# Optimization experiments

Measured on AMD Instinct MI355X. Metric: run time of the kernel, lower is better.

## Reference

```python
import jax, jax.numpy as jnp
import numpy as np

B, C, H, W = 4, 256, 224, 224
WH = WW = 8
SH = SW = 4
HEADS = 8
HD = C // HEADS
N = WH * WW
EPS = 1e-5


def _rel_index():
    coords = np.stack(np.meshgrid(np.arange(WH), np.arange(WW), indexing='ij')).reshape(2, -1)
    rel = (coords[:, :, None] - coords[:, None, :]).transpose(1, 2, 0).copy()
    rel[:, :, 0] += WH - 1
    rel[:, :, 1] += WW - 1
    rel[:, :, 0] *= 2 * WW - 1
    return rel.sum(-1)  # (N, N) int

REL_INDEX = _rel_index()


def _shift_mask(Hp, Wp):
    # Swin shift mask for one image: (nW, N, N) float, 0 or -100
    img = np.zeros((Hp, Wp))
    cnt = 0
    for a, b in [(0, Hp - WH), (Hp - WH, Hp - SH), (Hp - SH, Hp)]:
        for c, d in [(0, Wp - WW), (Wp - WW, Wp - SW), (Wp - SW, Wp)]:
            img[a:b, c:d] = cnt
            cnt += 1
    mw = img.reshape(Hp // WH, WH, Wp // WW, WW).transpose(0, 2, 1, 3).reshape(-1, N)
    diff = mw[:, None, :] - mw[:, :, None]  # [w, i, j] = mw[w,j] - mw[w,i]
    return np.where(diff != 0, np.float32(-100.0), np.float32(0.0)).astype(np.float32)


def _ln(x, w, b):
    m = jnp.mean(x, axis=-1, keepdims=True)
    v = jnp.mean(jnp.square(x - m), axis=-1, keepdims=True)
    return (x - m) * jax.lax.rsqrt(v + EPS) * w + b


def setup_inputs() -> dict:
    key = jax.random.key(0)
    ks = jax.random.split(key, 8)
    num_rel = (2 * WH - 1) * (2 * WW - 1)
    return {
        'x': jax.random.normal(ks[0], (B, C, H, W), dtype=jnp.float32),
        'qkv_w': jax.random.normal(ks[1], (3 * C, C), dtype=jnp.float32) * 0.02,
        'proj_w': jax.random.normal(ks[2], (C, C), dtype=jnp.float32) * 0.02,
        'proj_b': jnp.zeros((C,), dtype=jnp.float32),
        'rpb_table': jax.random.normal(ks[3], (num_rel, HEADS), dtype=jnp.float32) * 0.02,
        'norm1_w': jnp.ones((C,), dtype=jnp.float32),
        'norm1_b': jnp.zeros((C,), dtype=jnp.float32),
        'norm2_w': jnp.ones((C,), dtype=jnp.float32),
        'norm2_b': jnp.zeros((C,), dtype=jnp.float32),
        'mlp_w1': jax.random.normal(ks[4], (4 * C, C), dtype=jnp.float32) * 0.02,
        'mlp_b1': jnp.zeros((4 * C,), dtype=jnp.float32),
        'mlp_w2': jax.random.normal(ks[5], (C, 4 * C), dtype=jnp.float32) * 0.02,
        'mlp_b2': jnp.zeros((C,), dtype=jnp.float32),
    }


def reference(x, qkv_w, proj_w, proj_b, rpb_table, norm1_w, norm1_b,
              norm2_w, norm2_b, mlp_w1, mlp_b1, mlp_w2, mlp_b2):
    Bx, Cx, Hx, Wx = x.shape
    pad_h = (WH - Hx % WH) % WH
    pad_w = (WW - Wx % WW) % WW
    if pad_h or pad_w:
        x = jnp.pad(x, ((0, 0), (0, 0), (0, pad_h), (0, pad_w)))
    Hp, Wp = Hx + pad_h, Wx + pad_w
    x = jnp.transpose(x, (0, 2, 3, 1))                    # BHWC
    x = jnp.roll(x, (-SH, -SW), axis=(1, 2))
    nW = (Hp // WH) * (Wp // WW)
    # window partition -> (B*nW, N, C), batch-major
    xw = x.reshape(Bx, Hp // WH, WH, Wp // WW, WW, Cx)
    xw = jnp.transpose(xw, (0, 1, 3, 2, 4, 5)).reshape(-1, N, Cx)

    # ----- windowed attention -----
    h = _ln(xw, norm1_w, norm1_b)
    qkv = (h @ qkv_w.T).reshape(-1, N, 3, HEADS, HD)
    qkv = jnp.transpose(qkv, (2, 0, 3, 1, 4))             # (3, Bw, heads, N, hd)
    q, k, v = qkv[0], qkv[1], qkv[2]
    attn = jnp.einsum('bhnd,bhmd->bhnm', q, k) * (1.0 / HD ** 0.5)
    bias = jnp.transpose(rpb_table[REL_INDEX.reshape(-1)].reshape(N, N, HEADS), (2, 0, 1))
    attn = attn + bias[None]
    # faithful to torch: repeat_interleave(B, dim=0) -> window-major mask ordering
    mask = jnp.asarray(_shift_mask(Hp, Wp))               # (nW, N, N)
    attn = attn + jnp.repeat(mask, Bx, axis=0)[:, None]
    attn = jax.nn.softmax(attn, axis=-1)
    out = jnp.einsum('bhnm,bhmd->bhnd', attn, v)
    out = jnp.transpose(out, (0, 2, 1, 3)).reshape(-1, N, Cx)
    out = out @ proj_w.T + proj_b
    xw = xw + out

    # ----- MLP -----
    h = _ln(xw, norm2_w, norm2_b)
    h = jax.nn.gelu(h @ mlp_w1.T + mlp_b1, approximate=False) @ mlp_w2.T + mlp_b2
    xw = xw + h

    # window reverse, un-shift, un-pad
    x = xw.reshape(Bx, Hp // WH, Wp // WW, WH, WW, Cx)
    x = jnp.transpose(x, (0, 1, 3, 2, 4, 5)).reshape(Bx, Hp, Wp, Cx)
    x = jnp.roll(x, (SH, SW), axis=(1, 2))
    x = x[:, :Hx, :Wx, :]
    return jnp.transpose(x, (0, 3, 1, 2))
```

## Files before the change

### kernel.cpp

```cpp
#include <hip/hip_runtime.h>

typedef unsigned short u16;
typedef unsigned int   u32;
typedef __attribute__((ext_vector_type(8))) __bf16 bf16x8;
typedef __attribute__((ext_vector_type(4))) float  f32x4;
typedef __attribute__((ext_vector_type(4))) u16    u16x4;
typedef __attribute__((ext_vector_type(8))) u16    u16x8;

#define DEV __device__ __forceinline__

DEV u16 f2b(float f) {
  union { float f; u32 u; } a; a.f = f;
  const u32 u = a.u;
  return (u16)((u + 0x7fffu + ((u >> 16) & 1u)) >> 16);
}

DEV float gelu_fast(float x) {
  const float x2 = x * x;
  const float t  = __builtin_fmaf(0.1029430f, x2, 2.3022150f);
  const float e  = __builtin_exp2f(x * t);
  const float r  = __builtin_amdgcn_rcpf(1.0f + e);
  return __builtin_fmaf(-x, r, x);
}

DEV void gload16(const void* g, void* l) {
  __builtin_amdgcn_global_load_lds(
      (const __attribute__((address_space(1))) void*)g,
      (__attribute__((address_space(3))) void*)l, 16, 0, 0);
}

__global__ __launch_bounds__(256)
void conv_weights(const float* __restrict__ qkvw, const float* __restrict__ projw,
                  const float* __restrict__ w1,   const float* __restrict__ w2,
                  u16* __restrict__ dq, u16* __restrict__ dp,
                  u16* __restrict__ d1, u16* __restrict__ d2) {
  const int t = blockIdx.x * 256 + threadIdx.x;
  if (t < 196608)      dq[t]          = f2b(qkvw[t]);
  else if (t < 262144) dp[t - 196608] = f2b(projw[t - 196608]);
  else if (t < 524288) d1[t - 262144] = f2b(w1[t - 262144]);
  else                 d2[t - 524288] = f2b(w2[t - 524288]);
}

__global__ __launch_bounds__(256)
void ln1_win(const float* __restrict__ x, const float* __restrict__ w1,
             const float* __restrict__ b1, u16* __restrict__ hout,
             float* __restrict__ xwout) {
  __shared__ float xt[64 * 257];
  __shared__ float smean[256], srstd[256];
  const int tid = threadIdx.x, lane = tid & 63, wv = tid >> 6;
  const int g = blockIdx.x;
  const int b = g / 196, rem = g % 196;
  const int wh = rem / 7, wg = rem % 7;
  const int base_r = b * 784 + wh * 28 + wg * 4;
  const int pr = tid >> 5, pc = tid & 31;
  int hp = wh * 8 + 4 + pr; if (hp >= 224) hp -= 224;
  int wp = wg * 32 + 4 + pc; if (wp >= 224) wp -= 224;
  const long roff = (long)b * 256 * 50176 + hp * 224 + wp;

  float s = 0.f, q = 0.f;
  for (int cc = 0; cc < 4; ++cc) {
#pragma unroll 8
    for (int i = 0; i < 64; ++i) {
      const int c = cc * 64 + i;
      const float v = x[(long)c * 50176 + roff];
      xt[i * 257 + tid] = v;
      s += v; q += v * v;
    }
    __syncthreads();
#pragma unroll 8
    for (int jj = 0; jj < 64; ++jj) {
      const int p = jj * 4 + wv;
      const int m = (base_r + ((p & 31) >> 3)) * 64 + (p >> 5) * 8 + (p & 7);
      xwout[(long)m * 256 + cc * 64 + lane] = xt[lane * 257 + p];
    }
    __syncthreads();
  }
  const float mean = s * (1.f / 256.f);
  smean[tid] = mean;
  srstd[tid] = rsqrtf(q * (1.f / 256.f) - mean * mean + 1e-5f);
  __syncthreads();

  float wr_[4], br_[4];
#pragma unroll
  for (int cc = 0; cc < 4; ++cc) { wr_[cc] = w1[cc * 64 + lane]; br_[cc] = b1[cc * 64 + lane]; }
#pragma unroll 2
  for (int jj = 0; jj < 64; ++jj) {
    const int p = jj * 4 + wv;
    const int m = (base_r + ((p & 31) >> 3)) * 64 + (p >> 5) * 8 + (p & 7);
    const float mu = smean[p], rs = srstd[p];
#pragma unroll
    for (int cc = 0; cc < 4; ++cc) {
      const float v = xwout[(long)m * 256 + cc * 64 + lane];
      hout[(long)m * 256 + cc * 64 + lane] = f2b((v - mu) * rs * wr_[cc] + br_[cc]);
    }
  }
}

template<int EPI, int NCOL>
__global__ __launch_bounds__(512, 4)
void gemm_bt(const u16* __restrict__ A, const u16* __restrict__ Bw, const int K,
             float* __restrict__ fout, const float* __restrict__ bias,
             u16* __restrict__ bout,
             const float* __restrict__ lnw, const float* __restrict__ lnb,
             float* __restrict__ oout) {
  __shared__ __align__(16) u16 smem[24576];
  u16* sA0 = smem;
  u16* sB0 = smem + 4096;
  u16* sA1 = smem + 12288;
  u16* sB1 = smem + 16384;

  const int tid  = threadIdx.x;
  const int lane = tid & 63;
  const int wid  = tid >> 6;
  const int wrr  = wid >> 2;
  const int wcc  = wid & 3;

  const int nwg = gridDim.x;
  const int bid = blockIdx.x;
  const int wg  = (bid & 7) * (nwg >> 3) + (bid >> 3);
  const int row0 = wg * 128;

  const f32x4 vzero = {0.f, 0.f, 0.f, 0.f};

  const int l15  = lane & 15;
  const int l4   = lane >> 4;
  const int ksw2 = (l15 >> 1) & 3;
  const int lcol = (((tid & 3) ^ ((tid >> 3) & 3)) << 3);

  const u16* pA = A + (long)(row0 + (tid >> 2)) * K + lcol;
  const int wbase = wid * 512;

#define STAGE_TILE(KT, DA, DB)                  \
  {                                             \
    gload16(pA  + (KT), (DA) + wbase);          \
    gload16(pB  + (KT), (DB) + wbase);          \
    gload16(pB2 + (KT), (DB) + 4096 + wbase);   \
  }

#define COMPUTE_TILE(SA, SB, SWAP)                                                      \
  {                                                                                     \
    bf16x8 af[4], bfv[4];                                                               \
    _Pragma("unroll")                                                                   \
    for (int mi = 0; mi < 4; ++mi)                                                      \
      af[mi] = *(const bf16x8*)((SA) + (wrr * 64 + mi * 16 + l15) * 32 +                \
                                ((l4 ^ ksw2) << 3));                                    \
    _Pragma("unroll")                                                                   \
    for (int nj = 0; nj < 4; ++nj)                                                      \
      bfv[nj] = *(const bf16x8*)((SB) + (wcc * 64 + nj * 16 + l15) * 32 +               \
                                 ((l4 ^ ksw2) << 3));                                   \
    _Pragma("unroll")                                                                   \
    for (int mi = 0; mi < 4; ++mi)                                                      \
      _Pragma("unroll")                                                                 \
      for (int nj = 0; nj < 4; ++nj) {                                                  \
        if (SWAP)                                                                       \
          acc[mi][nj] = __builtin_amdgcn_mfma_f32_16x16x32_bf16(bfv[nj], af[mi],        \
                                                                acc[mi][nj], 0, 0, 0);  \
        else                                                                            \
          acc[mi][nj] = __builtin_amdgcn_mfma_f32_16x16x32_bf16(af[mi], bfv[nj],        \
                                                                acc[mi][nj], 0, 0, 0);  \
      }                                                                                 \
  }

#define KLOOP(SWAP)                                                  \
  {                                                                  \
    const int nt = K >> 5;                                           \
    STAGE_TILE(0, sA0, sB0);                                         \
    int cur = 0;                                                     \
    for (int t = 0; t < nt; ++t) {                                   \
      u16* cA = cur ? sA1 : sA0;                                     \
      u16* cB = cur ? sB1 : sB0;                                     \
      u16* nA = cur ? sA0 : sA1;                                     \
      u16* nB = cur ? sB0 : sB1;                                     \
      if (t + 1 < nt) {                                              \
        STAGE_TILE((t + 1) << 5, nA, nB);                            \
        asm volatile("s_waitcnt vmcnt(3)" ::: "memory");             \
      } else {                                                       \
        asm volatile("s_waitcnt vmcnt(0)" ::: "memory");             \
      }                                                              \
      __builtin_amdgcn_s_barrier();                                  \
      asm volatile("" ::: "memory");                                 \
      COMPUTE_TILE(cA, cB, SWAP);                                    \
      asm volatile("" ::: "memory");                                 \
      __builtin_amdgcn_s_barrier();                                  \
      cur ^= 1;                                                      \
    }                                                                \
  }

#pragma unroll
  for (int cb = 0; cb < NCOL; ++cb) {
    const int col0 = cb * 256;
    const u16* pB  = Bw + (long)(col0 + (tid >> 2)) * K + lcol;
    const u16* pB2 = pB + (long)128 * K;

    f32x4 acc[4][4];
#pragma unroll
    for (int i = 0; i < 4; ++i)
#pragma unroll
      for (int j = 0; j < 4; ++j) acc[i][j] = vzero;

    if (EPI == 0 && cb == 2) {
      KLOOP(0);
#pragma unroll
      for (int mi = 0; mi < 4; ++mi) {
        const int mb = row0 + wrr * 64 + mi * 16 + (l4 << 2);
        const int rrg = mb >> 6, ii = mb & 63;
#pragma unroll
        for (int nj = 0; nj < 4; ++nj) {
          const int n = 512 + wcc * 64 + nj * 16 + l15;
          const int hh = (n >> 5) & 7, d = n & 31;
          u16x4 p;
#pragma unroll
          for (int reg = 0; reg < 4; ++reg) p[reg] = f2b(acc[mi][nj][reg]);
          *(u16x4*)(bout + 102760448L + (long)((rrg * 8 + hh) * 32 + d) * 64 + ii) = p;
        }
      }
      continue;
    }

    KLOOP(1);

    if (EPI == 0) {
#pragma unroll
      for (int mi = 0; mi < 4; ++mi) {
        const int m = row0 + wrr * 64 + mi * 16 + l15;
        const int rr = m >> 6, ii = m & 63;
#pragma unroll
        for (int nj = 0; nj < 4; ++nj) {
          const int n = col0 + wcc * 64 + nj * 16 + (l4 << 2);
          const int s = n >> 8, hh = (n >> 5) & 7, d = n & 31;
          u16x4 p;
#pragma unroll
          for (int reg = 0; reg < 4; ++reg) p[reg] = f2b(acc[mi][nj][reg]);
          *(u16x4*)(bout + (long)s * 51380224L +
                    (long)((rr * 8 + hh) * 64 + ii) * 32 + d) = p;
        }
      }
    } else if (EPI == 1) {
      f32x4 b4[4];
#pragma unroll
      for (int nj = 0; nj < 4; ++nj)
        b4[nj] = *(const f32x4*)(bias + wcc * 64 + nj * 16 + (l4 << 2));
      float sS[4], sQ[4];
#pragma unroll
      for (int mi = 0; mi < 4; ++mi) {
        const int m = row0 + wrr * 64 + mi * 16 + l15;
        float* yrow = fout + (long)m * 256;
        float s = 0.f, q = 0.f;
#pragma unroll
        for (int nj = 0; nj < 4; ++nj) {
          const int n = wcc * 64 + nj * 16 + (l4 << 2);
          f32x4 o = *(f32x4*)(yrow + n);
#pragma unroll
          for (int reg = 0; reg < 4; ++reg) {
            o[reg] += acc[mi][nj][reg] + b4[nj][reg];
            s += o[reg]; q += o[reg] * o[reg];
          }
          *(f32x4*)(yrow + n) = o;
          acc[mi][nj] = o;
        }
        s += __shfl_xor(s, 16); s += __shfl_xor(s, 32);
        q += __shfl_xor(q, 16); q += __shfl_xor(q, 32);
        sS[mi] = s; sQ[mi] = q;
      }
      float* ps = (float*)smem;
      float* pq = ps + 512;
      __syncthreads();
      if (lane < 16) {
#pragma unroll
        for (int mi = 0; mi < 4; ++mi) {
          const int idx = (wrr * 64 + mi * 16 + l15) * 4 + wcc;
          ps[idx] = sS[mi]; pq[idx] = sQ[mi];
        }
      }
      __syncthreads();
#pragma unroll
      for (int mi = 0; mi < 4; ++mi) {
        const int m = row0 + wrr * 64 + mi * 16 + l15;
        const int base = (wrr * 64 + mi * 16 + l15) * 4;
        const float S = ps[base] + ps[base + 1] + ps[base + 2] + ps[base + 3];
        const float Q = pq[base] + pq[base + 1] + pq[base + 2] + pq[base + 3];
        const float mean = S * (1.f / 256.f);
        const float rstd = rsqrtf(Q * (1.f / 256.f) - mean * mean + 1e-5f);
#pragma unroll
        for (int nj = 0; nj < 4; ++nj) {
          const int n = wcc * 64 + nj * 16 + (l4 << 2);
          const f32x4 w4 = *(const f32x4*)(lnw + n);
          const f32x4 c4 = *(const f32x4*)(lnb + n);
          u16x4 p;
#pragma unroll
          for (int reg = 0; reg < 4; ++reg)
            p[reg] = f2b((acc[mi][nj][reg] - mean) * rstd * w4[reg] + c4[reg]);
          *(u16x4*)(bout + (long)m * 256 + n) = p;
        }
      }
    } else if (EPI == 3) {
      f32x4 b4[4];
#pragma unroll
      for (int nj = 0; nj < 4; ++nj)
        b4[nj] = *(const f32x4*)(bias + wcc * 64 + nj * 16 + (l4 << 2));
#pragma unroll
      for (int mi = 0; mi < 4; ++mi) {
        const int m = row0 + wrr * 64 + mi * 16 + l15;
        const float* yrow = fout + (long)m * 256;
#pragma unroll
        for (int nj = 0; nj < 4; ++nj) {
          const int n = wcc * 64 + nj * 16 + (l4 << 2);
          const f32x4 yv = *(const f32x4*)(yrow + n);
#pragma unroll
          for (int reg = 0; reg < 4; ++reg)
            acc[mi][nj][reg] += yv[reg] + b4[nj][reg];
        }
      }
      const int wr0 = row0 >> 6;
      const int b = wr0 / 784, rem = wr0 % 784;
      const int wh = rem / 28, wwb = rem % 28;
      float* tp = (float*)smem;
      const int pidx = tid & 127, cgrp = tid >> 7;
      const int pr = pidx >> 4, pc = pidx & 15;
      int hp = wh * 8 + 4 + pr;  if (hp >= 224) hp -= 224;
      int wp = wwb * 8 + 4 + pc; if (wp >= 224) wp -= 224;
      float* ob = oout + (long)b * 256 * 50176 + hp * 224 + wp;
#pragma unroll
      for (int cc = 0; cc < 4; ++cc) {
        __syncthreads();
        if (wcc == cc) {
#pragma unroll
          for (int mi = 0; mi < 4; ++mi) {
            const int ml = wrr * 64 + mi * 16 + l15;
            const int px = ((ml & 63) >> 3) * 16 + (ml >> 6) * 8 + (ml & 7);
#pragma unroll
            for (int nj = 0; nj < 4; ++nj)
#pragma unroll
              for (int reg = 0; reg < 4; ++reg)
                tp[(nj * 16 + (l4 << 2) + reg) * 128 + (px ^ (l4 << 2))] =
                    acc[mi][nj][reg];
          }
        }
        __syncthreads();
#pragma unroll 4
        for (int j = 0; j < 16; ++j) {
          const int cl = cgrp * 16 + j;
          ob[(long)(cc * 64 + cl) * 50176] =
              tp[cl * 128 + (pidx ^ (((cl >> 2) & 3) << 2))];
        }
      }
    } else if (EPI == 2) {
      f32x4 b4[4];
#pragma unroll
      for (int nj = 0; nj < 4; ++nj)
        b4[nj] = *(const f32x4*)(bias + col0 + wcc * 64 + nj * 16 + (l4 << 2));
#pragma unroll
      for (int mi = 0; mi < 4; ++mi) {
        const int m = row0 + wrr * 64 + mi * 16 + l15;
#pragma unroll
        for (int nj = 0; nj < 4; ++nj) {
          const int n = col0 + wcc * 64 + nj * 16 + (l4 << 2);
          u16x4 p;
#pragma unroll
          for (int reg = 0; reg < 4; ++reg)
            p[reg] = f2b(gelu_fast(acc[mi][nj][reg] + b4[nj][reg]));
          *(u16x4*)(bout + (long)m * 1024 + n) = p;
        }
      }
    }
  }

#undef STAGE_TILE
#undef COMPUTE_TILE
#undef KLOOP
}

__global__ __launch_bounds__(256)
void attn_win(const u16* __restrict__ qkv, const float* __restrict__ rpb,
              u16* __restrict__ aout) {
  __shared__ u16 Pl[4][4096];
  __shared__ float srpb[1800];
  const int tid = threadIdx.x, lane = tid & 63, wv = tid >> 6;
  const int bid = blockIdx.x;
  const int r = bid >> 1;
  const int h = (bid & 1) * 4 + wv;
  for (int i = tid; i < 1800; i += 256) srpb[i] = rpb[i];
  __syncthreads();

  const int midx = r >> 2;
  const int wh = midx / 28, ww = midx % 28;
  const int l15 = lane & 15, l4 = lane >> 4;

  u16* Pw = &Pl[wv][0];
  const long hb = (long)(r * 8 + h) * 2048;
  const u16* qh = qkv + hb;
  const u16* kh = qkv + 51380224 + hb;
  const u16* vh = qkv + 102760448 + hb;

  int rj[4], cj[4], labj[4];
#pragma unroll
  for (int nj = 0; nj < 4; ++nj) {
    const int j = nj * 16 + l15;
    rj[nj] = j >> 3; cj[nj] = j & 7;
    const int hp = wh * 8 + rj[nj], wp = ww * 8 + cj[nj];
    const int lh = (hp < 216) ? 0 : ((hp < 220) ? 1 : 2);
    const int lw = (wp < 216) ? 0 : ((wp < 220) ? 1 : 2);
    labj[nj] = lh * 3 + lw;
  }

  const f32x4 vzero = {0.f, 0.f, 0.f, 0.f};

  bf16x8 qf[4], kf[4];
#pragma unroll
  for (int mi = 0; mi < 4; ++mi)
    qf[mi] = *(const bf16x8*)(qh + (mi * 16 + l15) * 32 + l4 * 8);
#pragma unroll
  for (int nj = 0; nj < 4; ++nj)
    kf[nj] = *(const bf16x8*)(kh + (nj * 16 + l15) * 32 + l4 * 8);

  f32x4 S[4][4];
#pragma unroll
  for (int mi = 0; mi < 4; ++mi)
#pragma unroll
    for (int nj = 0; nj < 4; ++nj)
      S[mi][nj] = __builtin_amdgcn_mfma_f32_16x16x32_bf16(qf[mi], kf[nj], vzero, 0, 0, 0);

#pragma unroll
  for (int mi = 0; mi < 4; ++mi)
#pragma unroll
    for (int reg = 0; reg < 4; ++reg) {
      const int i = mi * 16 + (l4 << 2) + reg;
      const int ri = i >> 3, ci = i & 7;
      const int hp = wh * 8 + ri, wp = ww * 8 + ci;
      const int lh = (hp < 216) ? 0 : ((hp < 220) ? 1 : 2);
      const int lw = (wp < 216) ? 0 : ((wp < 220) ? 1 : 2);
      const int li = lh * 3 + lw;
      float v[4];
#pragma unroll
      for (int nj = 0; nj < 4; ++nj) {
        const int idx = (ri - rj[nj] + 7) * 15 + (ci - cj[nj] + 7);
        v[nj] = S[mi][nj][reg] * 0.17677669529663687f + srpb[idx * 8 + h]
              + ((li != labj[nj]) ? -100.0f : 0.0f);
      }
      float mx = fmaxf(fmaxf(v[0], v[1]), fmaxf(v[2], v[3]));
      mx = fmaxf(mx, __shfl_xor(mx, 1));
      mx = fmaxf(mx, __shfl_xor(mx, 2));
      mx = fmaxf(mx, __shfl_xor(mx, 4));
      mx = fmaxf(mx, __shfl_xor(mx, 8));
      float sum = 0.f;
#pragma unroll
      for (int nj = 0; nj < 4; ++nj) { v[nj] = __expf(v[nj] - mx); sum += v[nj]; }
      sum += __shfl_xor(sum, 1);
      sum += __shfl_xor(sum, 2);
      sum += __shfl_xor(sum, 4);
      sum += __shfl_xor(sum, 8);
      const float rinv = __builtin_amdgcn_rcpf(sum);
      const int sw = (i & 7) << 3;
#pragma unroll
      for (int nj = 0; nj < 4; ++nj)
        Pw[i * 64 + ((nj * 16 + l15) ^ sw)] = f2b(v[nj] * rinv);
    }

  f32x4 OT[2][4];
#pragma unroll
  for (int td = 0; td < 2; ++td)
#pragma unroll
    for (int ti = 0; ti < 4; ++ti) OT[td][ti] = vzero;

  const int rsw = (l15 & 7) << 3;
#pragma unroll
  for (int kk = 0; kk < 2; ++kk) {
    bf16x8 pf[4], vf[2];
#pragma unroll
    for (int ti = 0; ti < 4; ++ti)
      pf[ti] = *(const bf16x8*)(Pw + (ti * 16 + l15) * 64 + ((kk * 32 + l4 * 8) ^ rsw));
#pragma unroll
    for (int td = 0; td < 2; ++td)
      vf[td] = *(const bf16x8*)(vh + (td * 16 + l15) * 64 + kk * 32 + l4 * 8);
#pragma unroll
    for (int td = 0; td < 2; ++td)
#pragma unroll
      for (int ti = 0; ti < 4; ++ti)
        OT[td][ti] = __builtin_amdgcn_mfma_f32_16x16x32_bf16(vf[td], pf[ti], OT[td][ti], 0, 0, 0);
  }

#pragma unroll
  for (int td = 0; td < 2; ++td)
#pragma unroll
    for (int ti = 0; ti < 4; ++ti) {
      const int i = ti * 16 + l15;
      const int d0 = td * 16 + (l4 << 2);
      u16x4 p;
#pragma unroll
      for (int reg = 0; reg < 4; ++reg) p[reg] = f2b(OT[td][ti][reg]);
      *(u16x4*)(aout + (long)(r * 64 + i) * 256 + h * 32 + d0) = p;
    }
}

extern "C" void kernel_launch(void* const* d_in, const int* in_sizes, int n_in,
                              void* d_out, int out_size, void* d_ws, size_t ws_size,
                              hipStream_t stream) {
  (void)in_sizes; (void)n_in; (void)out_size; (void)ws_size;
  const float* x     = (const float*)d_in[0];
  const float* qkvw  = (const float*)d_in[1];
  const float* projw = (const float*)d_in[2];
  const float* projb = (const float*)d_in[3];
  const float* rpb   = (const float*)d_in[4];
  const float* n1w   = (const float*)d_in[5];
  const float* n1b   = (const float*)d_in[6];
  const float* n2w   = (const float*)d_in[7];
  const float* n2b   = (const float*)d_in[8];
  const float* w1    = (const float*)d_in[9];
  const float* b1    = (const float*)d_in[10];
  const float* w2    = (const float*)d_in[11];
  const float* b2    = (const float*)d_in[12];

  char* ws = (char*)d_ws;
  u16*   hbuf   = (u16*)(ws);
  u16*   qkvb   = (u16*)(ws + 102760448);
  u16*   abuf   = (u16*)(ws + 411041792);
  float* ybuf   = (float*)(ws + 513802240);
  u16*   hidb   = (u16*)(ws + 102760448);
  u16*   qkvwb  = (u16*)(ws + 719323136);
  u16*   projwb = (u16*)(ws + 719716352);
  u16*   w1b    = (u16*)(ws + 719847424);
  u16*   w2b    = (u16*)(ws + 720371712);

  conv_weights<<<3072, 256, 0, stream>>>(qkvw, projw, w1, w2, qkvwb, projwb, w1b, w2b);
  ln1_win<<<784, 256, 0, stream>>>(x, n1w, n1b, hbuf, ybuf);
  gemm_bt<0, 3><<<1568, 512, 0, stream>>>(hbuf, qkvwb, 256, nullptr, nullptr, qkvb, nullptr, nullptr, nullptr);
  attn_win<<<6272, 256, 0, stream>>>(qkvb, rpb, abuf);
  gemm_bt<1, 1><<<1568, 512, 0, stream>>>(abuf, projwb, 256, ybuf, projb, hbuf, n2w, n2b, nullptr);
  gemm_bt<2, 4><<<1568, 512, 0, stream>>>(hbuf, w1b, 256, nullptr, b1, hidb, nullptr, nullptr, nullptr);
  gemm_bt<3, 1><<<1568, 512, 0, stream>>>(hidb, w2b, 1024, ybuf, b2, nullptr, nullptr, nullptr, (float*)d_out);
}
```

Before: 1.145 ms.

## Fuse MLP fc1+GELU and fc2 into one kernel keeping hidden in LDS

```diff
diff --git a/kernel.cpp b/kernel.cpp
--- a/kernel.cpp
+++ b/kernel.cpp
@@ -5,7 +5,6 @@
 typedef __attribute__((ext_vector_type(8))) __bf16 bf16x8;
 typedef __attribute__((ext_vector_type(4))) float  f32x4;
 typedef __attribute__((ext_vector_type(4))) u16    u16x4;
-typedef __attribute__((ext_vector_type(8))) u16    u16x8;
 
 #define DEV __device__ __forceinline__
 
@@ -101,8 +100,7 @@
 void gemm_bt(const u16* __restrict__ A, const u16* __restrict__ Bw, const int K,
              float* __restrict__ fout, const float* __restrict__ bias,
              u16* __restrict__ bout,
-             const float* __restrict__ lnw, const float* __restrict__ lnb,
-             float* __restrict__ oout) {
+             const float* __restrict__ lnw, const float* __restrict__ lnb) {
   __shared__ __align__(16) u16 smem[24576];
   u16* sA0 = smem;
   u16* sB0 = smem + 4096;
@@ -293,81 +291,221 @@
           *(u16x4*)(bout + (long)m * 256 + n) = p;
         }
       }
-    } else if (EPI == 3) {
-      f32x4 b4[4];
-#pragma unroll
-      for (int nj = 0; nj < 4; ++nj)
-        b4[nj] = *(const f32x4*)(bias + wcc * 64 + nj * 16 + (l4 << 2));
-#pragma unroll
-      for (int mi = 0; mi < 4; ++mi) {
-        const int m = row0 + wrr * 64 + mi * 16 + l15;
-        const float* yrow = fout + (long)m * 256;
-#pragma unroll
-        for (int nj = 0; nj < 4; ++nj) {
-          const int n = wcc * 64 + nj * 16 + (l4 << 2);
-          const f32x4 yv = *(const f32x4*)(yrow + n);
-#pragma unroll
-          for (int reg = 0; reg < 4; ++reg)
-            acc[mi][nj][reg] += yv[reg] + b4[nj][reg];
-        }
-      }
-      const int wr0 = row0 >> 6;
-      const int b = wr0 / 784, rem = wr0 % 784;
-      const int wh = rem / 28, wwb = rem % 28;
-      float* tp = (float*)smem;
-      const int pidx = tid & 127, cgrp = tid >> 7;
-      const int pr = pidx >> 4, pc = pidx & 15;
-      int hp = wh * 8 + 4 + pr;  if (hp >= 224) hp -= 224;
-      int wp = wwb * 8 + 4 + pc; if (wp >= 224) wp -= 224;
-      float* ob = oout + (long)b * 256 * 50176 + hp * 224 + wp;
-#pragma unroll
-      for (int cc = 0; cc < 4; ++cc) {
-        __syncthreads();
-        if (wcc == cc) {
-#pragma unroll
-          for (int mi = 0; mi < 4; ++mi) {
-            const int ml = wrr * 64 + mi * 16 + l15;
-            const int px = ((ml & 63) >> 3) * 16 + (ml >> 6) * 8 + (ml & 7);
-#pragma unroll
-            for (int nj = 0; nj < 4; ++nj)
-#pragma unroll
-              for (int reg = 0; reg < 4; ++reg)
-                tp[(nj * 16 + (l4 << 2) + reg) * 128 + (px ^ (l4 << 2))] =
-                    acc[mi][nj][reg];
-          }
-        }
-        __syncthreads();
-#pragma unroll 4
-        for (int j = 0; j < 16; ++j) {
-          const int cl = cgrp * 16 + j;
-          ob[(long)(cc * 64 + cl) * 50176] =
-              tp[cl * 128 + (pidx ^ (((cl >> 2) & 3) << 2))];
-        }
-      }
-    } else if (EPI == 2) {
-      f32x4 b4[4];
-#pragma unroll
-      for (int nj = 0; nj < 4; ++nj)
-        b4[nj] = *(const f32x4*)(bias + col0 + wcc * 64 + nj * 16 + (l4 << 2));
-#pragma unroll
-      for (int mi = 0; mi < 4; ++mi) {
-        const int m = row0 + wrr * 64 + mi * 16 + l15;
-#pragma unroll
-        for (int nj = 0; nj < 4; ++nj) {
-          const int n = col0 + wcc * 64 + nj * 16 + (l4 << 2);
-          u16x4 p;
-#pragma unroll
-          for (int reg = 0; reg < 4; ++reg)
-            p[reg] = f2b(gelu_fast(acc[mi][nj][reg] + b4[nj][reg]));
-          *(u16x4*)(bout + (long)m * 1024 + n) = p;
-        }
-      }
-    }
-  }
-
+    }
+  }
 #undef STAGE_TILE
 #undef COMPUTE_TILE
 #undef KLOOP
+}
+
+__global__ __launch_bounds__(512, 2)
+void mlp_fused(const u16* __restrict__ A, const u16* __restrict__ w1b,
+               const u16* __restrict__ w2b, const float* __restrict__ y,
+               const float* __restrict__ b1, const float* __restrict__ b2,
+               float* __restrict__ oout) {
+  __shared__ __align__(16) u16 smem[57344];
+  u16* sA0 = smem;
+  u16* sB0 = smem + 4096;
+  u16* sA1 = smem + 12288;
+  u16* sB1 = smem + 16384;
+  u16* H   = smem + 24576;
+
+  const int tid  = threadIdx.x;
+  const int lane = tid & 63;
+  const int wid  = tid >> 6;
+  const int wrr  = wid >> 2;
+  const int wcc  = wid & 3;
+
+  const int nwg = gridDim.x;
+  const int bid = blockIdx.x;
+  const int wg  = (bid & 7) * (nwg >> 3) + (bid >> 3);
+  const int row0 = wg * 128;
+
+  const f32x4 vzero = {0.f, 0.f, 0.f, 0.f};
+  const int l15  = lane & 15;
+  const int l4   = lane >> 4;
+  const int ksw2 = (l15 >> 1) & 3;
+  const int lcol = (((tid & 3) ^ ((tid >> 3) & 3)) << 3);
+
+  const u16* pA = A + (long)(row0 + (tid >> 2)) * 256 + lcol;
+  const int wbase = wid * 512;
+
+  f32x4 acc2[4][4];
+#pragma unroll
+  for (int i = 0; i < 4; ++i)
+#pragma unroll
+    for (int j = 0; j < 4; ++j) acc2[i][j] = vzero;
+
+#define RD_FRAG(BUF, R0, OFF) \
+  (*(const bf16x8*)((BUF) + ((R0) + l15) * 32 + ((l4 ^ ksw2) << 3) + (OFF)))
+
+  for (int cb = 0; cb < 4; ++cb) {
+    const u16* pB  = w1b + (long)(cb * 256 + (tid >> 2)) * 256 + lcol;
+    const u16* pB2 = pB + 128 * 256;
+
+    f32x4 acc[4][4];
+#pragma unroll
+    for (int i = 0; i < 4; ++i)
+#pragma unroll
+      for (int j = 0; j < 4; ++j) acc[i][j] = vzero;
+
+    {
+      gload16(pA, sA0 + wbase);
+      gload16(pB, sB0 + wbase);
+      gload16(pB2, sB0 + 4096 + wbase);
+      int cur = 0;
+      for (int t = 0; t < 8; ++t) {
+        u16* cA = cur ? sA1 : sA0;
+        u16* cB = cur ? sB1 : sB0;
+        u16* nA = cur ? sA0 : sA1;
+        u16* nB = cur ? sB0 : sB1;
+        if (t + 1 < 8) {
+          const int kt = (t + 1) << 5;
+          gload16(pA + kt, nA + wbase);
+          gload16(pB + kt, nB + wbase);
+          gload16(pB2 + kt, nB + 4096 + wbase);
+          asm volatile("s_waitcnt vmcnt(3)" ::: "memory");
+        } else {
+          asm volatile("s_waitcnt vmcnt(0)" ::: "memory");
+        }
+        __builtin_amdgcn_s_barrier();
+        asm volatile("" ::: "memory");
+        {
+          bf16x8 af[4], bfv[4];
+#pragma unroll
+          for (int mi = 0; mi < 4; ++mi) af[mi] = RD_FRAG(cA, wrr * 64 + mi * 16, 0);
+#pragma unroll
+          for (int nj = 0; nj < 4; ++nj) bfv[nj] = RD_FRAG(cB, wcc * 64 + nj * 16, 0);
+#pragma unroll
+          for (int mi = 0; mi < 4; ++mi)
+#pragma unroll
+            for (int nj = 0; nj < 4; ++nj)
+              acc[mi][nj] = __builtin_amdgcn_mfma_f32_16x16x32_bf16(
+                  bfv[nj], af[mi], acc[mi][nj], 0, 0, 0);
+        }
+        asm volatile("" ::: "memory");
+        __builtin_amdgcn_s_barrier();
+        cur ^= 1;
+      }
+    }
+
+    {
+      f32x4 b4[4];
+#pragma unroll
+      for (int nj = 0; nj < 4; ++nj)
+        b4[nj] = *(const f32x4*)(b1 + cb * 256 + wcc * 64 + nj * 16 + (l4 << 2));
+#pragma unroll
+      for (int mi = 0; mi < 4; ++mi) {
+        const int m = wrr * 64 + mi * 16 + l15;
+#pragma unroll
+        for (int nj = 0; nj < 4; ++nj) {
+          u16x4 p;
+#pragma unroll
+          for (int reg = 0; reg < 4; ++reg)
+            p[reg] = f2b(gelu_fast(acc[mi][nj][reg] + b4[nj][reg]));
+          const int kt   = wcc * 2 + (nj >> 1);
+          const int slot = ((nj & 1) << 1) + (l4 >> 1);
+          *(u16x4*)(H + kt * 4096 + m * 32 +
+                    ((slot ^ ((m >> 1) & 3)) << 3) + ((l4 & 1) << 2)) = p;
+        }
+      }
+    }
+    __syncthreads();
+
+    {
+      const u16* qB  = w2b + (long)(tid >> 2) * 1024 + cb * 256 + lcol;
+      const u16* qB2 = qB + 128 * 1024;
+      gload16(qB, sB0 + wbase);
+      gload16(qB2, sB0 + 4096 + wbase);
+      int cur = 0;
+      for (int kt = 0; kt < 8; ++kt) {
+        u16* cB = cur ? sB1 : sB0;
+        u16* nB = cur ? sB0 : sB1;
+        if (kt + 1 < 8) {
+          const int ko = (kt + 1) << 5;
+          gload16(qB + ko, nB + wbase);
+          gload16(qB2 + ko, nB + 4096 + wbase);
+          asm volatile("s_waitcnt vmcnt(2)" ::: "memory");
+        } else {
+          asm volatile("s_waitcnt vmcnt(0)" ::: "memory");
+        }
+        __builtin_amdgcn_s_barrier();
+        asm volatile("" ::: "memory");
+        {
+          const u16* Hk = H + kt * 4096;
+          bf16x8 af[4], bfv[4];
+#pragma unroll
+          for (int mi = 0; mi < 4; ++mi) af[mi] = RD_FRAG(Hk, wrr * 64 + mi * 16, 0);
+#pragma unroll
+          for (int nj = 0; nj < 4; ++nj) bfv[nj] = RD_FRAG(cB, wcc * 64 + nj * 16, 0);
+#pragma unroll
+          for (int mi = 0; mi < 4; ++mi)
+#pragma unroll
+            for (int nj = 0; nj < 4; ++nj)
+              acc2[mi][nj] = __builtin_amdgcn_mfma_f32_16x16x32_bf16(
+                  bfv[nj], af[mi], acc2[mi][nj], 0, 0, 0);
+        }
+        asm volatile("" ::: "memory");
+        __builtin_amdgcn_s_barrier();
+        cur ^= 1;
+      }
+    }
+    __syncthreads();
+  }
+#undef RD_FRAG
+
+  {
+    f32x4 b4[4];
+#pragma unroll
+    for (int nj = 0; nj < 4; ++nj)
+      b4[nj] = *(const f32x4*)(b2 + wcc * 64 + nj * 16 + (l4 << 2));
+#pragma unroll
+    for (int mi = 0; mi < 4; ++mi) {
+      const int m = row0 + wrr * 64 + mi * 16 + l15;
+      const float* yrow = y + (long)m * 256;
+#pragma unroll
+      for (int nj = 0; nj < 4; ++nj) {
+        const int n = wcc * 64 + nj * 16 + (l4 << 2);
+        const f32x4 yv = *(const f32x4*)(yrow + n);
+#pragma unroll
+        for (int reg = 0; reg < 4; ++reg)
+          acc2[mi][nj][reg] += yv[reg] + b4[nj][reg];
+      }
+    }
+    const int wr0 = row0 >> 6;
+    const int b = wr0 / 784, rem = wr0 % 784;
+    const int wh = rem / 28, wwb = rem % 28;
+    float* tp = (float*)smem;
+    const int pidx = tid & 127, cgrp = tid >> 7;
+    const int pr = pidx >> 4, pc = pidx & 15;
+    int hp = wh * 8 + 4 + pr;  if (hp >= 224) hp -= 224;
+    int wp = wwb * 8 + 4 + pc; if (wp >= 224) wp -= 224;
+    float* ob = oout + (long)b * 256 * 50176 + hp * 224 + wp;
+#pragma unroll
+    for (int cc = 0; cc < 4; ++cc) {
+      __syncthreads();
+      if (wcc == cc) {
+#pragma unroll
+        for (int mi = 0; mi < 4; ++mi) {
+          const int ml = wrr * 64 + mi * 16 + l15;
+          const int px = ((ml & 63) >> 3) * 16 + (ml >> 6) * 8 + (ml & 7);
+#pragma unroll
+          for (int nj = 0; nj < 4; ++nj)
+#pragma unroll
+            for (int reg = 0; reg < 4; ++reg)
+              tp[(nj * 16 + (l4 << 2) + reg) * 128 + (px ^ (l4 << 2))] =
+                  acc2[mi][nj][reg];
+        }
+      }
+      __syncthreads();
+#pragma unroll 4
+      for (int j = 0; j < 16; ++j) {
+        const int cl = cgrp * 16 + j;
+        ob[(long)(cc * 64 + cl) * 50176] =
+            tp[cl * 128 + (pidx ^ (((cl >> 2) & 3) << 2))];
+      }
+    }
+  }
 }
 
 __global__ __launch_bounds__(256)
@@ -515,7 +653,6 @@
   u16*   qkvb   = (u16*)(ws + 102760448);
   u16*   abuf   = (u16*)(ws + 411041792);
   float* ybuf   = (float*)(ws + 513802240);
-  u16*   hidb   = (u16*)(ws + 102760448);
   u16*   qkvwb  = (u16*)(ws + 719323136);
   u16*   projwb = (u16*)(ws + 719716352);
   u16*   w1b    = (u16*)(ws + 719847424);
@@ -523,9 +660,8 @@
 
   conv_weights<<<3072, 256, 0, stream>>>(qkvw, projw, w1, w2, qkvwb, projwb, w1b, w2b);
   ln1_win<<<784, 256, 0, stream>>>(x, n1w, n1b, hbuf, ybuf);
-  gemm_bt<0, 3><<<1568, 512, 0, stream>>>(hbuf, qkvwb, 256, nullptr, nullptr, qkvb, nullptr, nullptr, nullptr);
+  gemm_bt<0, 3><<<1568, 512, 0, stream>>>(hbuf, qkvwb, 256, nullptr, nullptr, qkvb, nullptr, nullptr);
   attn_win<<<6272, 256, 0, stream>>>(qkvb, rpb, abuf);
-  gemm_bt<1, 1><<<1568, 512, 0, stream>>>(abuf, projwb, 256, ybuf, projb, hbuf, n2w, n2b, nullptr);
-  gemm_bt<2, 4><<<1568, 512, 0, stream>>>(hbuf, w1b, 256, nullptr, b1, hidb, nullptr, nullptr, nullptr);
-  gemm_bt<3, 1><<<1568, 512, 0, stream>>>(hidb, w2b, 1024, ybuf, b2, nullptr, nullptr, nullptr, (float*)d_out);
-}
+  gemm_bt<1, 1><<<1568, 512, 0, stream>>>(abuf, projwb, 256, ybuf, projb, hbuf, n2w, n2b);
+  mlp_fused<<<1568, 512, 0, stream>>>(hbuf, w1b, w2b, ybuf, b1, b2, (float*)d_out);
+}
```

New measurement: 1.063 ms. -7.2%, faster.
